# Kernel optimization log

Hardware: AMD Instinct MI355X
Metric: run time of the kernel (lower is better)

The kernel has to match this reference:

```python
import jax, jax.numpy as jnp
import numpy as np

CONTEXT_LENGTH = 2048
D_MODEL = 1024
N_HEADS = 16
D_HEAD = 64
ROPE_BASE = 10000.0
STD = 0.02


def rope(x, sines, cosines):
    # x: [b, s, h, d]; sines/cosines: [s, d//2]; interleaved even/odd pairing
    x_even = x[..., ::2]
    x_odd = x[..., 1::2]
    c = cosines[None, :, None, :]
    s = sines[None, :, None, :]
    out_even = x_even * c - x_odd * s
    out_odd = x_even * s + x_odd * c
    return jnp.stack((out_even, out_odd), axis=-1).reshape(x.shape)


def setup_inputs() -> dict:
    key = jax.random.key(0)
    k1, k2, k3, k4, k5 = jax.random.split(key, 5)
    x = jax.random.normal(k1, (2, 2048, D_MODEL), dtype=jnp.float32)
    key_weight = STD * jax.random.normal(k2, (N_HEADS, D_HEAD, D_MODEL), dtype=jnp.float32)
    query_weight = STD * jax.random.normal(k3, (N_HEADS, D_HEAD, D_MODEL), dtype=jnp.float32)
    value_weight = STD * jax.random.normal(k4, (N_HEADS, D_HEAD, D_MODEL), dtype=jnp.float32)
    output_weight = STD * jax.random.normal(k5, (D_MODEL, N_HEADS, D_HEAD), dtype=jnp.float32)
    angles = ROPE_BASE ** (-2.0 * jnp.arange(D_HEAD // 2, dtype=jnp.float32) / D_HEAD)
    positions = jnp.arange(CONTEXT_LENGTH, dtype=jnp.float32)
    apos = positions[:, None] * angles[None, :]  # [context, d_head//2]
    sines = jnp.sin(apos)
    cosines = jnp.cos(apos)
    return {"x": x, "key_weight": key_weight, "query_weight": query_weight,
            "value_weight": value_weight, "output_weight": output_weight,
            "sines": sines, "cosines": cosines}


def reference(x, key_weight, query_weight, value_weight, output_weight, sines, cosines):
    s = x.shape[1]
    sn, cs = sines[:s], cosines[:s]
    keys = jnp.einsum('hdm,bpm->bphd', key_weight, x)
    queries = jnp.einsum('hdm,bpm->bphd', query_weight, x)
    values = jnp.einsum('hdm,bpm->bphd', value_weight, x)
    keys = rope(keys, sn, cs)
    queries = rope(queries, sn, cs)
    # NOTE: no 1/sqrt(d_head) scaling, faithful to source
    scores = jnp.einsum('bkhd,bqhd->bhqk', keys, queries)
    mask = jnp.tril(jnp.ones((s, s), dtype=bool))  # causal (task='next_token')
    scores = jnp.where(mask[None, None], scores, -jnp.inf)
    pattern = jax.nn.softmax(scores, axis=-1)
    outputs = jnp.einsum('bhqk,bkhd->bqhd', pattern, values)
    return jnp.einsum('mhd,bphd->bpm', output_weight, outputs)
```

## Files before the change

### kernel.cpp

```cpp
#include <hip/hip_runtime.h>
#include <hip/hip_bf16.h>
#include <stdint.h>

typedef __bf16 bf16_t;
typedef bf16_t bf16x8 __attribute__((ext_vector_type(8)));
typedef float  f32x4  __attribute__((ext_vector_type(4)));

#define GAS __attribute__((address_space(1)))
#define LAS __attribute__((address_space(3)))

__device__ inline void gld_lds16(const void* g, void* l) {
    __builtin_amdgcn_global_load_lds((const GAS void*)g, (LAS void*)l, 16, 0, 0);
}

__device__ inline int swz(int row, int colbyte) {
    return row * 128 + (colbyte ^ ((row & 7) << 4));
}

__global__ __launch_bounds__(256) void k_cvt5(const float* __restrict__ i0, bf16_t* __restrict__ o0,
                                              const float* __restrict__ i1, bf16_t* __restrict__ o1,
                                              const float* __restrict__ i2, bf16_t* __restrict__ o2,
                                              const float* __restrict__ i3, bf16_t* __restrict__ o3,
                                              const float* __restrict__ i4, bf16_t* __restrict__ o4) {
    const float* in; bf16_t* out; int n;
    switch (blockIdx.y) {
        case 0: in = i0; out = o0; n = 4194304; break;
        case 1: in = i1; out = o1; n = 1048576; break;
        case 2: in = i2; out = o2; n = 1048576; break;
        case 3: in = i3; out = o3; n = 1048576; break;
        default: in = i4; out = o4; n = 1048576; break;
    }
    int i = (blockIdx.x * 256 + threadIdx.x) * 8;
    if (i >= n) return;
    f32x4 v0 = *(const f32x4*)(in + i);
    f32x4 v1 = *(const f32x4*)(in + i + 4);
    bf16x8 o;
    o[0] = (bf16_t)v0[0]; o[1] = (bf16_t)v0[1]; o[2] = (bf16_t)v0[2]; o[3] = (bf16_t)v0[3];
    o[4] = (bf16_t)v1[0]; o[5] = (bf16_t)v1[1]; o[6] = (bf16_t)v1[2]; o[7] = (bf16_t)v1[3];
    *(bf16x8*)(out + i) = o;
}

__global__ __launch_bounds__(256) void k_rope(bf16_t* __restrict__ Q, bf16_t* __restrict__ Kt,
                                              const float* __restrict__ sn,
                                              const float* __restrict__ cs) {
    int idx = blockIdx.x * 256 + threadIdx.x;
    bf16_t* T = blockIdx.y ? Kt : Q;
    int row = idx >> 9;
    int pi  = idx & 511;
    int h = pi >> 5, i = pi & 31;
    int p = row & 2047;
    float c = cs[p * 32 + i], s = sn[p * 32 + i];
    bf16_t* ptr = T + (size_t)row * 1024 + h * 64 + 2 * i;
    float e = (float)ptr[0], o = (float)ptr[1];
    ptr[0] = (bf16_t)(e * c - o * s);
    ptr[1] = (bf16_t)(e * s + o * c);
}

template <typename OutT>
__global__ __launch_bounds__(256) void k_gemm_bt(
    const bf16_t* __restrict__ A,
    const bf16_t* __restrict__ B0, const bf16_t* __restrict__ B1,
    OutT* __restrict__ C0, OutT* __restrict__ C1,
    int M, int N, int K) {
    const bf16_t* B = blockIdx.z == 0 ? B0 : B1;
    OutT*         C = blockIdx.z == 0 ? C0 : C1;
    const int BK = 32;
    __shared__ bf16_t As[128 * BK];
    __shared__ bf16_t Bs[128 * BK];
    int tid = threadIdx.x;
    int lane = tid & 63, wid = tid >> 6;
    int row0 = blockIdx.y * 128, col0 = blockIdx.x * 128;
    int wr = (wid >> 1) * 64, wc = (wid & 1) * 64;
    int lr = lane & 15, kg = lane >> 4;

    f32x4 acc[4][4];
#pragma unroll
    for (int i = 0; i < 4; ++i)
#pragma unroll
        for (int j = 0; j < 4; ++j) acc[i][j] = (f32x4){0.f, 0.f, 0.f, 0.f};

    int ob = tid * 16;
    for (int k0 = 0; k0 < K; k0 += BK) {
        __syncthreads();
#pragma unroll
        for (int p = 0; p < 2; ++p) {
            int off = p * 4096 + ob;
            int r = off >> 6;
            int cb = off & 63;
            gld_lds16((const char*)A + ((size_t)(row0 + r) * K + k0) * 2 + cb, (char*)As + off);
            gld_lds16((const char*)B + ((size_t)(col0 + r) * K + k0) * 2 + cb, (char*)Bs + off);
        }
        __syncthreads();
        bf16x8 af[4], bfr[4];
#pragma unroll
        for (int mi = 0; mi < 4; ++mi)
            af[mi] = *(const bf16x8*)&As[(wr + mi * 16 + lr) * BK + kg * 8];
#pragma unroll
        for (int ni = 0; ni < 4; ++ni)
            bfr[ni] = *(const bf16x8*)&Bs[(wc + ni * 16 + lr) * BK + kg * 8];
#pragma unroll
        for (int mi = 0; mi < 4; ++mi)
#pragma unroll
            for (int ni = 0; ni < 4; ++ni)
                acc[mi][ni] = __builtin_amdgcn_mfma_f32_16x16x32_bf16(af[mi], bfr[ni],
                                                                      acc[mi][ni], 0, 0, 0);
    }
#pragma unroll
    for (int mi = 0; mi < 4; ++mi)
#pragma unroll
        for (int ni = 0; ni < 4; ++ni)
#pragma unroll
            for (int r = 0; r < 4; ++r) {
                int row = row0 + wr + mi * 16 + kg * 4 + r;
                int col = col0 + wc + ni * 16 + lr;
                C[(size_t)row * N + col] = (OutT)acc[mi][ni][r];
            }
}

__global__ __launch_bounds__(256) void k_flash(const bf16_t* __restrict__ Q,
                                               const bf16_t* __restrict__ K,
                                               const bf16_t* __restrict__ Vt,
                                               bf16_t* __restrict__ Ob) {
    const int DM = 1024, S = 2048, NB = 4096;
    int h = blockIdx.y, b = blockIdx.z;
    int tid = threadIdx.x, lane = tid & 63, wid = tid >> 6;
    int lr = lane & 15, kg = lane >> 4;
    int rowbase = b * S;
    int colbase = h * 64;
    int j = blockIdx.x * 4 + wid;

    __shared__ bf16_t Ps[4][32 * 64];
    char* Pw = (char*)&Ps[wid][0];

    const bf16_t* Kg = K + (size_t)rowbase * DM + colbase;
    const bf16_t* Vg = Vt + (size_t)colbase * NB + rowbase;

#define LOADK(kb, dst)                                                               \
    _Pragma("unroll") for (int ni = 0; ni < 4; ++ni)                                 \
    _Pragma("unroll") for (int s2 = 0; s2 < 2; ++s2)                                 \
        dst[ni * 2 + s2] =                                                           \
            *(const bf16x8*)&Kg[(size_t)((kb) * 64 + ni * 16 + lr) * DM + s2 * 32 + kg * 8];

#define LOADV(kb, dst)                                                               \
    _Pragma("unroll") for (int ni = 0; ni < 4; ++ni)                                 \
    _Pragma("unroll") for (int s2 = 0; s2 < 2; ++s2)                                 \
        dst[ni * 2 + s2] =                                                           \
            *(const bf16x8*)&Vg[(size_t)(ni * 16 + lr) * NB + (kb) * 64 + s2 * 32 + kg * 8];

#define STEP(kb, kf, vf, kfN, vfN)                                                   \
    {                                                                                \
        f32x4 sa[2][4];                                                              \
        _Pragma("unroll") for (int mi = 0; mi < 2; ++mi)                             \
        _Pragma("unroll") for (int ni = 0; ni < 4; ++ni)                             \
            sa[mi][ni] = (f32x4){0.f, 0.f, 0.f, 0.f};                                \
        _Pragma("unroll") for (int s2 = 0; s2 < 2; ++s2)                             \
        _Pragma("unroll") for (int ni = 0; ni < 4; ++ni)                             \
        _Pragma("unroll") for (int mi = 0; mi < 2; ++mi)                             \
            sa[mi][ni] = __builtin_amdgcn_mfma_f32_16x16x32_bf16(                    \
                qf[mi][s2], kf[ni * 2 + s2], sa[mi][ni], 0, 0, 0);                   \
        if ((kb) < kbmax) { LOADK((kb) + 1, kfN); }                                  \
        if ((kb) == kbmax) {                    \
            _Pragma("unroll") for (int mi = 0; mi < 2; ++mi)                         \
            _Pragma("unroll") for (int ni = 0; ni < 4; ++ni)                         \
            _Pragma("unroll") for (int r = 0; r < 4; ++r)                            \
                if ((kb) * 64 + ni * 16 + lr > spos + mi * 16 + kg * 4 + r)          \
                    sa[mi][ni][r] = -1e30f;                                          \
        }                                                                            \
        _Pragma("unroll") for (int mi = 0; mi < 2; ++mi)                             \
        _Pragma("unroll") for (int r = 0; r < 4; ++r) {                              \
            float mx = fmaxf(fmaxf(sa[mi][0][r], sa[mi][1][r]),                      \
                             fmaxf(sa[mi][2][r], sa[mi][3][r]));                     \
            _Pragma("unroll") for (int off = 1; off < 16; off <<= 1)                 \
                mx = fmaxf(mx, __shfl_xor(mx, off));                                 \
            float mo = m_run[mi][r];                                                 \
            float mn = fmaxf(mo, mx);                                                \
            float sc = __expf(mo - mn);                                              \
            float rs = 0.f;                                                          \
            _Pragma("unroll") for (int ni = 0; ni < 4; ++ni) {                       \
                float pv = __expf(sa[mi][ni][r] - mn);                               \
                sa[mi][ni][r] = pv;                                                  \
                rs += pv;                                                            \
            }                                                                        \
            _Pragma("unroll") for (int off = 1; off < 16; off <<= 1)                 \
                rs += __shfl_xor(rs, off);                                           \
            l_run[mi][r] = l_run[mi][r] * sc + rs;                                   \
            m_run[mi][r] = mn;                                                       \
            _Pragma("unroll") for (int ni = 0; ni < 4; ++ni) Oa[mi][ni][r] *= sc;    \
        }                                                                            \
        _Pragma("unroll") for (int mi = 0; mi < 2; ++mi)                             \
        _Pragma("unroll") for (int r = 0; r < 4; ++r)                                \
        _Pragma("unroll") for (int ni = 0; ni < 4; ++ni)                             \
            *(bf16_t*)(Pw + swz(mi * 16 + kg * 4 + r, (ni * 16 + lr) * 2)) =         \
                (bf16_t)sa[mi][ni][r];                                               \
        _Pragma("unroll") for (int s2 = 0; s2 < 2; ++s2) {                           \
            bf16x8 pf0 = *(const bf16x8*)(Pw + swz(lr, s2 * 64 + kg * 16));          \
            bf16x8 pf1 = *(const bf16x8*)(Pw + swz(16 + lr, s2 * 64 + kg * 16));     \
            _Pragma("unroll") for (int ni = 0; ni < 4; ++ni) {                       \
                Oa[0][ni] = __builtin_amdgcn_mfma_f32_16x16x32_bf16(                 \
                    pf0, vf[ni * 2 + s2], Oa[0][ni], 0, 0, 0);                       \
                Oa[1][ni] = __builtin_amdgcn_mfma_f32_16x16x32_bf16(                 \
                    pf1, vf[ni * 2 + s2], Oa[1][ni], 0, 0, 0);                       \
            }                                                                        \
        }                                                                            \
        if ((kb) < kbmax) { LOADV((kb) + 1, vfN); }                                  \
    }

#pragma unroll 1
    for (int half = 0; half < 2; ++half) {
        int s = half ? (63 - j) : j;
        int spos = s * 32;
        int kbmax = s >> 1;

        bf16x8 qf[2][2];
#pragma unroll
        for (int mi = 0; mi < 2; ++mi)
#pragma unroll
            for (int s2 = 0; s2 < 2; ++s2)
                qf[mi][s2] = *(const bf16x8*)&Q[(size_t)(rowbase + spos + mi * 16 + lr) * DM +
                                                colbase + s2 * 32 + kg * 8];

        f32x4 Oa[2][4];
        float m_run[2][4], l_run[2][4];
#pragma unroll
        for (int mi = 0; mi < 2; ++mi)
#pragma unroll
            for (int ni = 0; ni < 4; ++ni) Oa[mi][ni] = (f32x4){0.f, 0.f, 0.f, 0.f};
#pragma unroll
        for (int mi = 0; mi < 2; ++mi)
#pragma unroll
            for (int r = 0; r < 4; ++r) { m_run[mi][r] = -1e30f; l_run[mi][r] = 0.f; }

        bf16x8 kfA[8], kfB[8], vfA[8], vfB[8];
        LOADK(0, kfA);
        LOADV(0, vfA);
#pragma unroll 1
        for (int kb = 0; kb <= kbmax; kb += 2) {
            STEP(kb, kfA, vfA, kfB, vfB);
            if (kb + 1 <= kbmax) STEP(kb + 1, kfB, vfB, kfA, vfA);
        }

#pragma unroll
        for (int mi = 0; mi < 2; ++mi)
#pragma unroll
            for (int r = 0; r < 4; ++r) {
                float inv = 1.f / l_run[mi][r];
                size_t row = (size_t)(rowbase + spos + mi * 16 + kg * 4 + r);
#pragma unroll
                for (int ni = 0; ni < 4; ++ni)
                    Ob[row * DM + colbase + ni * 16 + lr] = (bf16_t)(Oa[mi][ni][r] * inv);
            }
    }
#undef LOADK
#undef LOADV
#undef STEP
}

extern "C" void kernel_launch(void* const* d_in, const int* in_sizes, int n_in,
                              void* d_out, int out_size, void* d_ws, size_t ws_size,
                              hipStream_t stream) {
    const float* x  = (const float*)d_in[0];
    const float* wk = (const float*)d_in[1];
    const float* wq = (const float*)d_in[2];
    const float* wv = (const float*)d_in[3];
    const float* wo = (const float*)d_in[4];
    const float* sn = (const float*)d_in[5];
    const float* cs = (const float*)d_in[6];
    float* out = (float*)d_out;
    (void)in_sizes; (void)n_in; (void)out_size; (void)ws_size;

    char* ws = (char*)d_ws;
    const size_t MB = 1024 * 1024;
    bf16_t* xb  = (bf16_t*)(ws + 0);
    bf16_t* wqb = (bf16_t*)(ws + 8 * MB);
    bf16_t* wkb = (bf16_t*)(ws + 10 * MB);
    bf16_t* wvb = (bf16_t*)(ws + 12 * MB);
    bf16_t* wob = (bf16_t*)(ws + 14 * MB);
    bf16_t* Qb  = (bf16_t*)(ws + 16 * MB);
    bf16_t* Kb  = (bf16_t*)(ws + 24 * MB);
    bf16_t* Vtb = (bf16_t*)(ws + 32 * MB);
    bf16_t* Ob  = (bf16_t*)(ws + 40 * MB);

    k_cvt5<<<dim3(2048, 5), 256, 0, stream>>>(x, xb, wq, wqb, wk, wkb, wv, wvb, wo, wob);

    k_gemm_bt<bf16_t><<<dim3(8, 32, 2), 256, 0, stream>>>(
        xb, wqb, wkb, Qb, Kb, 4096, 1024, 1024);
    k_gemm_bt<bf16_t><<<dim3(32, 8, 1), 256, 0, stream>>>(
        wvb, xb, xb, Vtb, Vtb, 1024, 4096, 1024);

    k_rope<<<dim3(8192, 2), 256, 0, stream>>>(Qb, Kb, sn, cs);

    k_flash<<<dim3(8, 16, 2), 256, 0, stream>>>(Qb, Kb, Vtb, Ob);

    k_gemm_bt<float><<<dim3(8, 32, 1), 256, 0, stream>>>(
        Ob, wob, wob, out, out, 4096, 1024, 1024);
}
```

Before: 192.1 us.

## Transpose flash-attention MFMA operands and spread query tiles across more blocks

The flash kernel now computes S^T = K·Q^T with swapped MFMA operands, so each lane owns one query row and row reductions need only two cross-lane shuffles instead of four-step butterflies. P and O are written as packed bf16x4 vectors. The causal load balancing that paired tile j with 63-j inside one wave is replaced by one query tile per wave across a doubled grid with launch_bounds(256,2), and the double-buffered K/V register sets are collapsed to one set to lower register pressure. Per-wave work is now uneven across the causal triangle, which the scheduler has to absorb through the extra blocks and higher occupancy.

```diff
diff --git a/kernel.cpp b/kernel.cpp
--- a/kernel.cpp
+++ b/kernel.cpp
@@ -3,6 +3,7 @@
 #include <stdint.h>
 
 typedef __bf16 bf16_t;
+typedef bf16_t bf16x4 __attribute__((ext_vector_type(4)));
 typedef bf16_t bf16x8 __attribute__((ext_vector_type(8)));
 typedef float  f32x4  __attribute__((ext_vector_type(4)));
 
@@ -117,17 +118,19 @@
             }
 }
 
-__global__ __launch_bounds__(256) void k_flash(const bf16_t* __restrict__ Q,
-                                               const bf16_t* __restrict__ K,
-                                               const bf16_t* __restrict__ Vt,
-                                               bf16_t* __restrict__ Ob) {
+__global__ __launch_bounds__(256, 2) void k_flash(const bf16_t* __restrict__ Q,
+                                                  const bf16_t* __restrict__ K,
+                                                  const bf16_t* __restrict__ Vt,
+                                                  bf16_t* __restrict__ Ob) {
     const int DM = 1024, S = 2048, NB = 4096;
     int h = blockIdx.y, b = blockIdx.z;
     int tid = threadIdx.x, lane = tid & 63, wid = tid >> 6;
     int lr = lane & 15, kg = lane >> 4;
     int rowbase = b * S;
     int colbase = h * 64;
-    int j = blockIdx.x * 4 + wid;
+    int s = wid * 16 + blockIdx.x;
+    int spos = s * 32;
+    int kbmax = s >> 1;
 
     __shared__ bf16_t Ps[4][32 * 64];
     char* Pw = (char*)&Ps[wid][0];
@@ -142,117 +145,128 @@
             *(const bf16x8*)&Kg[(size_t)((kb) * 64 + ni * 16 + lr) * DM + s2 * 32 + kg * 8];
 
 #define LOADV(kb, dst)                                                               \
-    _Pragma("unroll") for (int ni = 0; ni < 4; ++ni)                                 \
+    _Pragma("unroll") for (int nd = 0; nd < 4; ++nd)                                 \
     _Pragma("unroll") for (int s2 = 0; s2 < 2; ++s2)                                 \
-        dst[ni * 2 + s2] =                                                           \
-            *(const bf16x8*)&Vg[(size_t)(ni * 16 + lr) * NB + (kb) * 64 + s2 * 32 + kg * 8];
-
-#define STEP(kb, kf, vf, kfN, vfN)                                                   \
-    {                                                                                \
-        f32x4 sa[2][4];                                                              \
-        _Pragma("unroll") for (int mi = 0; mi < 2; ++mi)                             \
-        _Pragma("unroll") for (int ni = 0; ni < 4; ++ni)                             \
-            sa[mi][ni] = (f32x4){0.f, 0.f, 0.f, 0.f};                                \
-        _Pragma("unroll") for (int s2 = 0; s2 < 2; ++s2)                             \
-        _Pragma("unroll") for (int ni = 0; ni < 4; ++ni)                             \
-        _Pragma("unroll") for (int mi = 0; mi < 2; ++mi)                             \
-            sa[mi][ni] = __builtin_amdgcn_mfma_f32_16x16x32_bf16(                    \
-                qf[mi][s2], kf[ni * 2 + s2], sa[mi][ni], 0, 0, 0);                   \
-        if ((kb) < kbmax) { LOADK((kb) + 1, kfN); }                                  \
-        if ((kb) == kbmax) {                    \
-            _Pragma("unroll") for (int mi = 0; mi < 2; ++mi)                         \
-            _Pragma("unroll") for (int ni = 0; ni < 4; ++ni)                         \
-            _Pragma("unroll") for (int r = 0; r < 4; ++r)                            \
-                if ((kb) * 64 + ni * 16 + lr > spos + mi * 16 + kg * 4 + r)          \
-                    sa[mi][ni][r] = -1e30f;                                          \
-        }                                                                            \
-        _Pragma("unroll") for (int mi = 0; mi < 2; ++mi)                             \
-        _Pragma("unroll") for (int r = 0; r < 4; ++r) {                              \
-            float mx = fmaxf(fmaxf(sa[mi][0][r], sa[mi][1][r]),                      \
-                             fmaxf(sa[mi][2][r], sa[mi][3][r]));                     \
-            _Pragma("unroll") for (int off = 1; off < 16; off <<= 1)                 \
-                mx = fmaxf(mx, __shfl_xor(mx, off));                                 \
-            float mo = m_run[mi][r];                                                 \
-            float mn = fmaxf(mo, mx);                                                \
-            float sc = __expf(mo - mn);                                              \
-            float rs = 0.f;                                                          \
-            _Pragma("unroll") for (int ni = 0; ni < 4; ++ni) {                       \
-                float pv = __expf(sa[mi][ni][r] - mn);                               \
-                sa[mi][ni][r] = pv;                                                  \
-                rs += pv;                                                            \
-            }                                                                        \
-            _Pragma("unroll") for (int off = 1; off < 16; off <<= 1)                 \
-                rs += __shfl_xor(rs, off);                                           \
-            l_run[mi][r] = l_run[mi][r] * sc + rs;                                   \
-            m_run[mi][r] = mn;                                                       \
-            _Pragma("unroll") for (int ni = 0; ni < 4; ++ni) Oa[mi][ni][r] *= sc;    \
-        }                                                                            \
-        _Pragma("unroll") for (int mi = 0; mi < 2; ++mi)                             \
-        _Pragma("unroll") for (int r = 0; r < 4; ++r)                                \
-        _Pragma("unroll") for (int ni = 0; ni < 4; ++ni)                             \
-            *(bf16_t*)(Pw + swz(mi * 16 + kg * 4 + r, (ni * 16 + lr) * 2)) =         \
-                (bf16_t)sa[mi][ni][r];                                               \
-        _Pragma("unroll") for (int s2 = 0; s2 < 2; ++s2) {                           \
-            bf16x8 pf0 = *(const bf16x8*)(Pw + swz(lr, s2 * 64 + kg * 16));          \
-            bf16x8 pf1 = *(const bf16x8*)(Pw + swz(16 + lr, s2 * 64 + kg * 16));     \
-            _Pragma("unroll") for (int ni = 0; ni < 4; ++ni) {                       \
-                Oa[0][ni] = __builtin_amdgcn_mfma_f32_16x16x32_bf16(                 \
-                    pf0, vf[ni * 2 + s2], Oa[0][ni], 0, 0, 0);                       \
-                Oa[1][ni] = __builtin_amdgcn_mfma_f32_16x16x32_bf16(                 \
-                    pf1, vf[ni * 2 + s2], Oa[1][ni], 0, 0, 0);                       \
-            }                                                                        \
-        }                                                                            \
-        if ((kb) < kbmax) { LOADV((kb) + 1, vfN); }                                  \
-    }
+        dst[nd * 2 + s2] =                                                           \
+            *(const bf16x8*)&Vg[(size_t)(nd * 16 + lr) * NB + (kb) * 64 + s2 * 32 + kg * 8];
+
+    bf16x8 qf[2][2];
+#pragma unroll
+    for (int mi = 0; mi < 2; ++mi)
+#pragma unroll
+        for (int s2 = 0; s2 < 2; ++s2)
+            qf[mi][s2] = *(const bf16x8*)&Q[(size_t)(rowbase + spos + mi * 16 + lr) * DM +
+                                            colbase + s2 * 32 + kg * 8];
+
+    f32x4 Oa[2][4];
+    float m_run[2], l_run[2];
+#pragma unroll
+    for (int mi = 0; mi < 2; ++mi) {
+        m_run[mi] = -1e30f;
+        l_run[mi] = 0.f;
+#pragma unroll
+        for (int nd = 0; nd < 4; ++nd) Oa[mi][nd] = (f32x4){0.f, 0.f, 0.f, 0.f};
+    }
+
+    bf16x8 kf[8], vf[8];
+    LOADK(0, kf);
+    LOADV(0, vf);
 
 #pragma unroll 1
-    for (int half = 0; half < 2; ++half) {
-        int s = half ? (63 - j) : j;
-        int spos = s * 32;
-        int kbmax = s >> 1;
-
-        bf16x8 qf[2][2];
+    for (int kb = 0; kb <= kbmax; ++kb) {
+        f32x4 sa[2][4];
 #pragma unroll
         for (int mi = 0; mi < 2; ++mi)
 #pragma unroll
-            for (int s2 = 0; s2 < 2; ++s2)
-                qf[mi][s2] = *(const bf16x8*)&Q[(size_t)(rowbase + spos + mi * 16 + lr) * DM +
-                                                colbase + s2 * 32 + kg * 8];
-
-        f32x4 Oa[2][4];
-        float m_run[2][4], l_run[2][4];
-#pragma unroll
-        for (int mi = 0; mi < 2; ++mi)
-#pragma unroll
-            for (int ni = 0; ni < 4; ++ni) Oa[mi][ni] = (f32x4){0.f, 0.f, 0.f, 0.f};
-#pragma unroll
-        for (int mi = 0; mi < 2; ++mi)
-#pragma unroll
-            for (int r = 0; r < 4; ++r) { m_run[mi][r] = -1e30f; l_run[mi][r] = 0.f; }
-
-        bf16x8 kfA[8], kfB[8], vfA[8], vfB[8];
-        LOADK(0, kfA);
-        LOADV(0, vfA);
-#pragma unroll 1
-        for (int kb = 0; kb <= kbmax; kb += 2) {
-            STEP(kb, kfA, vfA, kfB, vfB);
-            if (kb + 1 <= kbmax) STEP(kb + 1, kfB, vfB, kfA, vfA);
-        }
-
-#pragma unroll
-        for (int mi = 0; mi < 2; ++mi)
-#pragma unroll
-            for (int r = 0; r < 4; ++r) {
-                float inv = 1.f / l_run[mi][r];
-                size_t row = (size_t)(rowbase + spos + mi * 16 + kg * 4 + r);
+            for (int ni = 0; ni < 4; ++ni) sa[mi][ni] = (f32x4){0.f, 0.f, 0.f, 0.f};
+#pragma unroll
+        for (int s2 = 0; s2 < 2; ++s2)
+#pragma unroll
+            for (int ni = 0; ni < 4; ++ni)
+#pragma unroll
+                for (int mi = 0; mi < 2; ++mi)
+                    sa[mi][ni] = __builtin_amdgcn_mfma_f32_16x16x32_bf16(
+                        kf[ni * 2 + s2], qf[mi][s2], sa[mi][ni], 0, 0, 0);
+
+        bool pre = kb < kbmax;
+        if (pre) { LOADK(kb + 1, kf); }
+
+        if (kb == kbmax) {
+#pragma unroll
+            for (int mi = 0; mi < 2; ++mi) {
+                int qpos = spos + mi * 16 + lr;
 #pragma unroll
                 for (int ni = 0; ni < 4; ++ni)
-                    Ob[row * DM + colbase + ni * 16 + lr] = (bf16_t)(Oa[mi][ni][r] * inv);
-            }
+#pragma unroll
+                    for (int r = 0; r < 4; ++r)
+                        if (kb * 64 + ni * 16 + kg * 4 + r > qpos) sa[mi][ni][r] = -1e30f;
+            }
+        }
+
+#pragma unroll
+        for (int mi = 0; mi < 2; ++mi) {
+            float mx = -1e30f;
+#pragma unroll
+            for (int ni = 0; ni < 4; ++ni)
+                mx = fmaxf(mx, fmaxf(fmaxf(sa[mi][ni][0], sa[mi][ni][1]),
+                                     fmaxf(sa[mi][ni][2], sa[mi][ni][3])));
+            mx = fmaxf(mx, __shfl_xor(mx, 16));
+            mx = fmaxf(mx, __shfl_xor(mx, 32));
+            float mo = m_run[mi];
+            float mn = fmaxf(mo, mx);
+            float sc = __expf(mo - mn);
+            m_run[mi] = mn;
+            float rs = 0.f;
+#pragma unroll
+            for (int ni = 0; ni < 4; ++ni) {
+                bf16x4 pk;
+#pragma unroll
+                for (int r = 0; r < 4; ++r) {
+                    float pv = __expf(sa[mi][ni][r] - mn);
+                    rs += pv;
+                    pk[r] = (bf16_t)pv;
+                }
+                *(bf16x4*)(Pw + swz(mi * 16 + lr, (ni * 16 + kg * 4) * 2)) = pk;
+            }
+            rs += __shfl_xor(rs, 16);
+            rs += __shfl_xor(rs, 32);
+            l_run[mi] = l_run[mi] * sc + rs;
+#pragma unroll
+            for (int nd = 0; nd < 4; ++nd) {
+                Oa[mi][nd][0] *= sc; Oa[mi][nd][1] *= sc;
+                Oa[mi][nd][2] *= sc; Oa[mi][nd][3] *= sc;
+            }
+        }
+
+#pragma unroll
+        for (int mi = 0; mi < 2; ++mi) {
+#pragma unroll
+            for (int s2 = 0; s2 < 2; ++s2) {
+                bf16x8 pf = *(const bf16x8*)(Pw + swz(mi * 16 + lr, s2 * 64 + kg * 16));
+#pragma unroll
+                for (int nd = 0; nd < 4; ++nd)
+                    Oa[mi][nd] = __builtin_amdgcn_mfma_f32_16x16x32_bf16(
+                        vf[nd * 2 + s2], pf, Oa[mi][nd], 0, 0, 0);
+            }
+        }
+
+        if (pre) { LOADV(kb + 1, vf); }
+    }
+
+#pragma unroll
+    for (int mi = 0; mi < 2; ++mi) {
+        float inv = 1.f / l_run[mi];
+        size_t row = (size_t)(rowbase + spos + mi * 16 + lr);
+#pragma unroll
+        for (int nd = 0; nd < 4; ++nd) {
+            bf16x4 o;
+#pragma unroll
+            for (int r = 0; r < 4; ++r) o[r] = (bf16_t)(Oa[mi][nd][r] * inv);
+            *(bf16x4*)&Ob[row * DM + colbase + nd * 16 + kg * 4] = o;
+        }
     }
 #undef LOADK
 #undef LOADV
-#undef STEP
 }
 
 extern "C" void kernel_launch(void* const* d_in, const int* in_sizes, int n_in,
@@ -289,7 +303,7 @@
 
     k_rope<<<dim3(8192, 2), 256, 0, stream>>>(Qb, Kb, sn, cs);
 
-    k_flash<<<dim3(8, 16, 2), 256, 0, stream>>>(Qb, Kb, Vtb, Ob);
+    k_flash<<<dim3(16, 16, 2), 256, 0, stream>>>(Qb, Kb, Vtb, Ob);
 
     k_gemm_bt<float><<<dim3(8, 32, 1), 256, 0, stream>>>(
         Ob, wob, wob, out, out, 4096, 1024, 1024);
```

After: 179.0 us. -6.8%, faster.
